# Kernel tuning notes

Measured on AMD Instinct MI355X. Metric: run time of the kernel, lower is better.

## Reference

```python
import jax, jax.numpy as jnp
import numpy as np


def setup_inputs() -> dict:
    key = jax.random.key(0)
    k1, k2 = jax.random.split(key)
    pred = jax.random.normal(k1, (4, 8192, 3), dtype=jnp.float32)
    gt = jax.random.normal(k2, (4, 8192, 3), dtype=jnp.float32)
    return {"pred": pred, "gt": gt}


def reference(pred, gt):
    # pairwise squared distances: [B, N, M]
    diff = pred[:, :, None, :] - gt[:, None, :, :]
    distances = jnp.sum(diff ** 2, axis=-1)
    pred_to_gt = jnp.min(distances, axis=2)  # [B, N]
    gt_to_pred = jnp.min(distances, axis=1)  # [B, M]
    return jnp.mean(pred_to_gt) + jnp.mean(gt_to_pred)
```

## Files before the change

### kernel.cpp

```cpp
#include <hip/hip_runtime.h>
#include <math.h>


typedef _Float16 half8 __attribute__((ext_vector_type(8)));
typedef float f32x16 __attribute__((ext_vector_type(16)));

#define NPTS   8192
#define CLOUD  32768
#define NQ_TOT 65536
#define TT     512
#define NTC    16
#define GRID   4096

#define TLO 0
#define THI 1
#define QLO 2
#define QHI 3

__device__ __forceinline__ void split2(float v, _Float16& h, _Float16& l) {
  h = (_Float16)v; l = (_Float16)(v - (float)h);
}

__device__ __forceinline__ float min_fold(float m, const f32x16& d) {
  float a = fminf(fminf(d[0], d[1]), d[2]);
  float b = fminf(fminf(d[3], d[4]), d[5]);
  float c = fminf(fminf(d[6], d[7]), d[8]);
  float e = fminf(fminf(d[9], d[10]), d[11]);
  float f = fminf(fminf(d[12], d[13]), d[14]);
  float g = fminf(fminf(a, b), c);
  float h = fminf(fminf(e, f), d[15]);
  return fminf(m, fminf(g, h));
}

__global__ __launch_bounds__(256) void pack_kernel(
    const float* __restrict__ pred, const float* __restrict__ gt,
    half8* __restrict__ planes, float* __restrict__ out) {
  int i = blockIdx.x * 256 + threadIdx.x;
  int cloud = i >> 15, j = i & (CLOUD - 1);
  const float* src = cloud ? gt : pred;
  float x = src[3 * j], y = src[3 * j + 1], z = src[3 * j + 2];
  float s = x * x + y * y + z * z;
  _Float16 xh, xl, yh, yl, zh, zl, sh, sl;
  split2(x, xh, xl); split2(y, yh, yl); split2(z, zh, zl); split2(s, sh, sl);
  _Float16 Xh = (_Float16)(-2.f * (float)xh), Xl = (_Float16)(-2.f * (float)xl);
  _Float16 Yh = (_Float16)(-2.f * (float)yh), Yl = (_Float16)(-2.f * (float)yl);
  _Float16 Zh = (_Float16)(-2.f * (float)zh), Zl = (_Float16)(-2.f * (float)zl);
  _Float16 one = (_Float16)1.0f;
  planes[(size_t)TLO * NQ_TOT + i] = (half8){Xh, Xl, Xh, Xl, Yh, Yl, Yh, Yl};
  planes[(size_t)THI * NQ_TOT + i] = (half8){Zh, Zl, Zh, Zl, sh, sl, one, one};
  planes[(size_t)QLO * NQ_TOT + i] = (half8){xh, xh, xl, xl, yh, yh, yl, yl};
  planes[(size_t)QHI * NQ_TOT + i] = (half8){zh, zh, zl, zl, one, one, sh, sl};
  if (i == 0) out[0] = 0.f;
}

__global__ __launch_bounds__(256, 6) void chamfer_mfma(
    const half8* __restrict__ planes, unsigned int* __restrict__ minbits) {
  __shared__ __align__(16) half8 lds0[TT];
  __shared__ __align__(16) half8 lds1[TT];

  int bid = blockIdx.x;
  int tc   = bid & (NTC - 1);
  int qblk = (bid >> 4) & 31;
  int b    = (bid >> 9) & 3;
  int dir  = bid >> 11;
  int t = threadIdx.x, lane = t & 63, wave = t >> 6;

  size_t tbase = (size_t)(dir ? 0 : CLOUD) + b * NPTS + tc * TT;
  size_t qbase = (size_t)(dir ? CLOUD : 0) + b * NPTS + qblk * 256 + wave * 64;

  lds0[t]       = planes[(size_t)TLO * NQ_TOT + tbase + t];
  lds0[t + 256] = planes[(size_t)TLO * NQ_TOT + tbase + t + 256];
  lds1[t]       = planes[(size_t)THI * NQ_TOT + tbase + t];
  lds1[t + 256] = planes[(size_t)THI * NQ_TOT + tbase + t + 256];

  int hi = lane >> 5;
  size_t qoff = (size_t)(hi ? QHI : QLO) * NQ_TOT + qbase + (lane & 31);
  half8 bq0 = planes[qoff];
  half8 bq1 = planes[qoff + 32];
  __syncthreads();

  const half8* abase = hi ? &lds1[lane & 31] : &lds0[lane & 31];
  float m0 = INFINITY, m1 = INFINITY;
  f32x16 zero = {};
  #pragma unroll 2
  for (int g = 0; g < TT / 32; ++g) {
    half8 a = abase[g * 32];
    f32x16 d0 = __builtin_amdgcn_mfma_f32_32x32x16_f16(a, bq0, zero, 0, 0, 0);
    f32x16 d1 = __builtin_amdgcn_mfma_f32_32x32x16_f16(a, bq1, zero, 0, 0, 0);
    m0 = min_fold(m0, d0);
    m1 = min_fold(m1, d1);
  }
  m0 = fminf(m0, __shfl_xor(m0, 32, 64));
  m1 = fminf(m1, __shfl_xor(m1, 32, 64));

  if (lane < 32) {
    size_t qi = (size_t)dir * CLOUD + b * NPTS + qblk * 256 + wave * 64 + (lane & 31);
    atomicMin(&minbits[qi],      __float_as_uint(fmaxf(m0, 0.f)));
    atomicMin(&minbits[qi + 32], __float_as_uint(fmaxf(m1, 0.f)));
  }
}

__global__ __launch_bounds__(256) void reduce_kernel(
    const unsigned int* __restrict__ minbits, float* __restrict__ out) {
  __shared__ float wsum[4];
  float acc = 0.f;
  for (int i = blockIdx.x * 256 + threadIdx.x; i < NQ_TOT; i += 64 * 256)
    acc += __uint_as_float(minbits[i]);
  acc *= (1.0f / 32768.0f);
  #pragma unroll
  for (int off = 32; off > 0; off >>= 1) acc += __shfl_down(acc, off, 64);
  int wid = threadIdx.x >> 6;
  if ((threadIdx.x & 63) == 0) wsum[wid] = acc;
  __syncthreads();
  if (threadIdx.x == 0) atomicAdd(out, wsum[0] + wsum[1] + wsum[2] + wsum[3]);
}

extern "C" void kernel_launch(void* const* d_in, const int* in_sizes, int n_in,
                              void* d_out, int out_size, void* d_ws, size_t ws_size,
                              hipStream_t stream) {
  const float* pred = (const float*)d_in[0];
  const float* gt   = (const float*)d_in[1];
  float* out = (float*)d_out;
  half8* planes = (half8*)d_ws;
  unsigned int* minbits = (unsigned int*)((char*)d_ws + 4u * NQ_TOT * 16);

  pack_kernel<<<256, 256, 0, stream>>>(pred, gt, planes, out);
  chamfer_mfma<<<GRID, 256, 0, stream>>>(planes, minbits);
  reduce_kernel<<<64, 256, 0, stream>>>(minbits, out);
}
```

Before: 79.68 us.

## Load target tiles directly from global with register prefetch, double target tile size

Drops the LDS staging and the __syncthreads. Each wave now reads its target half8 operands straight from global memory (L2/L1), software-prefetching the next two groups into registers while the MFMAs run. The target tile per block grows from 512 to 1024, which halves the grid and the number of atomicMin updates per query. In exchange, target data is re-read from global by every wave instead of once per block, and there are fewer blocks to fill the GPU.

```diff
diff --git a/kernel.cpp b/kernel.cpp
--- a/kernel.cpp
+++ b/kernel.cpp
@@ -8,9 +8,9 @@
 #define NPTS   8192
 #define CLOUD  32768
 #define NQ_TOT 65536
-#define TT     512
-#define NTC    16
-#define GRID   4096
+#define TT     1024
+#define NTC    8
+#define GRID   2048
 
 #define TLO 0
 #define THI 1
@@ -55,40 +55,50 @@
 
 __global__ __launch_bounds__(256, 6) void chamfer_mfma(
     const half8* __restrict__ planes, unsigned int* __restrict__ minbits) {
-  __shared__ __align__(16) half8 lds0[TT];
-  __shared__ __align__(16) half8 lds1[TT];
-
   int bid = blockIdx.x;
   int tc   = bid & (NTC - 1);
-  int qblk = (bid >> 4) & 31;
-  int b    = (bid >> 9) & 3;
-  int dir  = bid >> 11;
+  int qblk = (bid >> 3) & 31;
+  int b    = (bid >> 8) & 3;
+  int dir  = bid >> 10;
   int t = threadIdx.x, lane = t & 63, wave = t >> 6;
 
   size_t tbase = (size_t)(dir ? 0 : CLOUD) + b * NPTS + tc * TT;
   size_t qbase = (size_t)(dir ? CLOUD : 0) + b * NPTS + qblk * 256 + wave * 64;
 
-  lds0[t]       = planes[(size_t)TLO * NQ_TOT + tbase + t];
-  lds0[t + 256] = planes[(size_t)TLO * NQ_TOT + tbase + t + 256];
-  lds1[t]       = planes[(size_t)THI * NQ_TOT + tbase + t];
-  lds1[t + 256] = planes[(size_t)THI * NQ_TOT + tbase + t + 256];
-
   int hi = lane >> 5;
+  const half8* ap = planes + (size_t)(hi ? THI : TLO) * NQ_TOT + tbase + (lane & 31);
   size_t qoff = (size_t)(hi ? QHI : QLO) * NQ_TOT + qbase + (lane & 31);
   half8 bq0 = planes[qoff];
   half8 bq1 = planes[qoff + 32];
-  __syncthreads();
 
-  const half8* abase = hi ? &lds1[lane & 31] : &lds0[lane & 31];
   float m0 = INFINITY, m1 = INFINITY;
   f32x16 zero = {};
+
+  half8 a0 = ap[0];
+  half8 a1 = ap[32];
   #pragma unroll 2
-  for (int g = 0; g < TT / 32; ++g) {
-    half8 a = abase[g * 32];
-    f32x16 d0 = __builtin_amdgcn_mfma_f32_32x32x16_f16(a, bq0, zero, 0, 0, 0);
-    f32x16 d1 = __builtin_amdgcn_mfma_f32_32x32x16_f16(a, bq1, zero, 0, 0, 0);
+  for (int g = 0; g < TT / 32 - 2; g += 2) {
+    half8 n0 = ap[(g + 2) * 32];
+    half8 n1 = ap[(g + 3) * 32];
+    f32x16 d0 = __builtin_amdgcn_mfma_f32_32x32x16_f16(a0, bq0, zero, 0, 0, 0);
+    f32x16 d1 = __builtin_amdgcn_mfma_f32_32x32x16_f16(a0, bq1, zero, 0, 0, 0);
     m0 = min_fold(m0, d0);
     m1 = min_fold(m1, d1);
+    f32x16 e0 = __builtin_amdgcn_mfma_f32_32x32x16_f16(a1, bq0, zero, 0, 0, 0);
+    f32x16 e1 = __builtin_amdgcn_mfma_f32_32x32x16_f16(a1, bq1, zero, 0, 0, 0);
+    m0 = min_fold(m0, e0);
+    m1 = min_fold(m1, e1);
+    a0 = n0; a1 = n1;
+  }
+  {
+    f32x16 d0 = __builtin_amdgcn_mfma_f32_32x32x16_f16(a0, bq0, zero, 0, 0, 0);
+    f32x16 d1 = __builtin_amdgcn_mfma_f32_32x32x16_f16(a0, bq1, zero, 0, 0, 0);
+    m0 = min_fold(m0, d0);
+    m1 = min_fold(m1, d1);
+    f32x16 e0 = __builtin_amdgcn_mfma_f32_32x32x16_f16(a1, bq0, zero, 0, 0, 0);
+    f32x16 e1 = __builtin_amdgcn_mfma_f32_32x32x16_f16(a1, bq1, zero, 0, 0, 0);
+    m0 = min_fold(m0, e0);
+    m1 = min_fold(m1, e1);
   }
   m0 = fminf(m0, __shfl_xor(m0, 32, 64));
   m1 = fminf(m1, __shfl_xor(m1, 32, 64));
```

After: 78.75 us. About the same (-1.2%).
